# Kernel tuning notes

Hardware: AMD Instinct MI355X
Metric: run time of the kernel (lower is better)

Reference implementation:

```python
import jax, jax.numpy as jnp
import numpy as np

H, W = 480, 640          # sensor resolution (self.dim)
N = 16_777_216           # number of events


def setup_inputs() -> dict:
    key = jax.random.key(0)
    k1, k2, k3, k4 = jax.random.split(key, 4)
    x = jax.random.randint(k1, (N,), 0, W).astype(jnp.float32)
    y = jax.random.randint(k2, (N,), 0, H).astype(jnp.float32)
    t = jax.random.uniform(k3, (N,), minval=1e-3, maxval=1.0)
    p = jax.random.randint(k4, (N,), 0, 2).astype(jnp.float32) * 2.0 - 1.0  # {-1, +1}
    events = jnp.stack([x, y, t, p], axis=1)  # [N, 4]
    return {"events": events}


def reference(events):
    # events: [N, 4] columns (x, y, t, p)
    x, y, t, p = events.T
    t = t / t.max()          # computed in original (unused for indexing)
    p = (p + 1.0) / 2.0      # {-1,1} -> {0,1}
    idx = (x + W * y + W * H * p).astype(jnp.int32)  # [N] flat voxel index
    # scatter-add event counts, then binarize (vox_ec[vox_ec > 0] = 1)
    vox = jnp.zeros(2 * H * W, dtype=events.dtype).at[idx].add(jnp.ones_like(x))
    vox = jnp.where(vox > 0, jnp.ones_like(vox), vox)
    return vox.reshape(-1, 2, H, W)  # [1, 2, H, W]
```

## Files before the change

kernel.cpp:

```cpp
#include <hip/hip_runtime.h>
#include <hip/hip_bf16.h>

#define EW 640
#define EH 480
#define NVOX (2 * EH * EW)
#define NWORDS (NVOX / 32)
#define BLK 512

typedef float vf4 __attribute__((ext_vector_type(4)));

__device__ __forceinline__ int ev_idx(vf4 e) {
    float p01 = (e.w + 1.0f) * 0.5f;
    return (int)(e.x + (float)EW * e.y + (float)(EW * EH) * p01);
}

__global__ void __launch_bounds__(BLK, 4)
event_bitmap_kernel(const vf4* __restrict__ events,
                    unsigned int* __restrict__ gbm, int n) {
    __shared__ unsigned int bm[NWORDS];
    for (int w = threadIdx.x; w < NWORDS; w += BLK) bm[w] = 0u;
    __syncthreads();

    const int nth = gridDim.x * BLK;
    int i = blockIdx.x * BLK + threadIdx.x;
    for (; i + 3 * nth < n; i += 4 * nth) {
        vf4 e0 = events[i];
        vf4 e1 = events[i + nth];
        vf4 e2 = events[i + 2 * nth];
        vf4 e3 = events[i + 3 * nth];
        int x0 = ev_idx(e0), x1 = ev_idx(e1), x2 = ev_idx(e2), x3 = ev_idx(e3);
        atomicOr(&bm[x0 >> 5], 1u << (x0 & 31));
        atomicOr(&bm[x1 >> 5], 1u << (x1 & 31));
        atomicOr(&bm[x2 >> 5], 1u << (x2 & 31));
        atomicOr(&bm[x3 >> 5], 1u << (x3 & 31));
    }
    for (; i < n; i += nth) {
        vf4 e = events[i];
        int x = ev_idx(e);
        atomicOr(&bm[x >> 5], 1u << (x & 31));
    }
    __syncthreads();

    for (int w = threadIdx.x; w < NWORDS; w += BLK) {
        unsigned int v = bm[w];
        if (v) atomicOr(&gbm[w], v);
    }
}

__global__ void __launch_bounds__(256)
expand_kernel(const unsigned int* __restrict__ gbm, float* __restrict__ out) {
    int i = blockIdx.x * 256 + threadIdx.x;
    if (i < NVOX) {
        unsigned int wv = gbm[i >> 5];
        out[i] = ((wv >> (i & 31)) & 1u) ? 1.0f : 0.0f;
    }
}

extern "C" void kernel_launch(void* const* d_in, const int* in_sizes, int n_in,
                              void* d_out, int out_size, void* d_ws, size_t ws_size,
                              hipStream_t stream) {
    const vf4* events = (const vf4*)d_in[0];
    unsigned int* gbm = (unsigned int*)d_ws;
    float* out = (float*)d_out;
    int n = in_sizes[0] / 4;

    hipMemsetAsync(gbm, 0, NWORDS * sizeof(unsigned int), stream);

    event_bitmap_kernel<<<512, BLK, 0, stream>>>(events, gbm, n);
    expand_kernel<<<(NVOX + 255) / 256, 256, 0, stream>>>(gbm, out);
}
```

Before: 372.4 us.

## Replace global atomic bitmap merge with per-block bitmaps and tree OR reduction

Result: no change. 369.3 us (-0.8%).

```diff
diff --git a/kernel.cpp b/kernel.cpp
--- a/kernel.cpp
+++ b/kernel.cpp
@@ -6,6 +6,8 @@
 #define NVOX (2 * EH * EW)
 #define NWORDS (NVOX / 32)
 #define BLK 512
+#define NBLOCKS 512
+#define NCHUNK 8
 
 typedef float vf4 __attribute__((ext_vector_type(4)));
 
@@ -16,7 +18,7 @@
 
 __global__ void __launch_bounds__(BLK, 4)
 event_bitmap_kernel(const vf4* __restrict__ events,
-                    unsigned int* __restrict__ gbm, int n) {
+                    unsigned int* __restrict__ bms, int n) {
     __shared__ unsigned int bm[NWORDS];
     for (int w = threadIdx.x; w < NWORDS; w += BLK) bm[w] = 0u;
     __syncthreads();
@@ -41,18 +43,40 @@
     }
     __syncthreads();
 
-    for (int w = threadIdx.x; w < NWORDS; w += BLK) {
-        unsigned int v = bm[w];
-        if (v) atomicOr(&gbm[w], v);
-    }
+    uint4* dst = (uint4*)(bms + (size_t)blockIdx.x * NWORDS);
+    const uint4* src = (const uint4*)bm;
+    for (int w = threadIdx.x; w < NWORDS / 4; w += BLK) dst[w] = src[w];
 }
 
 __global__ void __launch_bounds__(256)
-expand_kernel(const unsigned int* __restrict__ gbm, float* __restrict__ out) {
-    int i = blockIdx.x * 256 + threadIdx.x;
-    if (i < NVOX) {
-        unsigned int wv = gbm[i >> 5];
-        out[i] = ((wv >> (i & 31)) & 1u) ? 1.0f : 0.0f;
+reduce_kernel(const unsigned int* __restrict__ bms,
+              unsigned int* __restrict__ partial) {
+    int w = blockIdx.x * 256 + threadIdx.x;
+    int b0 = blockIdx.y * (NBLOCKS / NCHUNK);
+    unsigned int acc = 0u;
+    #pragma unroll 8
+    for (int b = 0; b < NBLOCKS / NCHUNK; ++b)
+        acc |= bms[(size_t)(b0 + b) * NWORDS + w];
+    partial[(size_t)blockIdx.y * NWORDS + w] = acc;
+}
+
+__global__ void __launch_bounds__(256)
+expand_kernel(const unsigned int* __restrict__ partial,
+              float* __restrict__ out) {
+    int w = blockIdx.x * 256 + threadIdx.x;
+    unsigned int acc = 0u;
+    #pragma unroll
+    for (int c = 0; c < NCHUNK; ++c)
+        acc |= partial[(size_t)c * NWORDS + w];
+    vf4* dst = (vf4*)(out + (size_t)w * 32);
+    #pragma unroll
+    for (int q = 0; q < 8; ++q) {
+        vf4 v;
+        v.x = (acc >> (q * 4 + 0)) & 1u ? 1.0f : 0.0f;
+        v.y = (acc >> (q * 4 + 1)) & 1u ? 1.0f : 0.0f;
+        v.z = (acc >> (q * 4 + 2)) & 1u ? 1.0f : 0.0f;
+        v.w = (acc >> (q * 4 + 3)) & 1u ? 1.0f : 0.0f;
+        dst[q] = v;
     }
 }
 
@@ -60,12 +84,13 @@
                               void* d_out, int out_size, void* d_ws, size_t ws_size,
                               hipStream_t stream) {
     const vf4* events = (const vf4*)d_in[0];
-    unsigned int* gbm = (unsigned int*)d_ws;
     float* out = (float*)d_out;
     int n = in_sizes[0] / 4;
 
-    hipMemsetAsync(gbm, 0, NWORDS * sizeof(unsigned int), stream);
+    unsigned int* bms = (unsigned int*)d_ws;
+    unsigned int* partial = bms + (size_t)NBLOCKS * NWORDS;
 
-    event_bitmap_kernel<<<512, BLK, 0, stream>>>(events, gbm, n);
-    expand_kernel<<<(NVOX + 255) / 256, 256, 0, stream>>>(gbm, out);
+    event_bitmap_kernel<<<NBLOCKS, BLK, 0, stream>>>(events, bms, n);
+    reduce_kernel<<<dim3(NWORDS / 256, NCHUNK), 256, 0, stream>>>(bms, partial);
+    expand_kernel<<<NWORDS / 256, 256, 0, stream>>>(partial, out);
 }
```
